# Optimization experiments

Hardware: AMD Instinct MI355X
Metric: run time of the kernel (lower is better)

Reference implementation:

```python
import jax, jax.numpy as jnp
import numpy as np

BSZ, L, P, H = 8, 8192, 128, 128


def setup_inputs() -> dict:
    key = jax.random.key(0)
    ks = jax.random.split(key, 7)
    x = jax.random.normal(ks[0], (BSZ, L, H), jnp.float32)
    A_diag = jax.random.uniform(ks[1], (P,), jnp.float32, 0.0, 2.0)
    G_diag = jax.random.uniform(ks[2], (P,), jnp.float32, 0.0, 1.0)
    dt = jax.random.normal(ks[3], (P,), jnp.float32)
    B = jax.random.uniform(ks[4], (P, H, 2), jnp.float32, -1.0, 1.0) / np.sqrt(H)
    C = jax.random.uniform(ks[5], (H, P, 2), jnp.float32, -1.0, 1.0) / np.sqrt(P)
    D = jax.random.normal(ks[6], (H,), jnp.float32)
    return {"x": x, "A_diag": A_diag, "G_diag": G_diag, "dt": dt, "B": B, "C": C, "D": D}


def _project_G(G, A, dt):
    # clamp G >= 0 and fold A into the valid stability interval [A_low, A_high]
    G = jnp.maximum(G, 0.0)
    dt2 = jnp.maximum(dt ** 2, 1e-06)
    s = jnp.sqrt(1.0 + dt * G)
    A_low = (2.0 + dt * G - 2.0 * s) / dt2
    A_high = (2.0 + dt * G + 2.0 * s) / dt2
    A_proj = A_low + jax.nn.relu(A - A_low) - jax.nn.relu(A - A_high)
    return A_proj, G


def _binop(q_i, q_j):
    # 2x2 block (per diagonal state p) recurrence composition: M_j @ M_i
    A_i, b_i = q_i
    A_j, b_j = q_j
    A_new = jnp.einsum('...ikp,...kjp->...ijp', A_j, A_i)
    b_new = jnp.einsum('...ikp,...kp->...ip', A_j, b_i) + b_j
    return A_new, b_new


def reference(x, A_diag, G_diag, dt, B, C, D):
    # _project_A_dt
    dt_s = jax.nn.sigmoid(dt)                       # (P,)
    A = jnp.maximum(A_diag, 0.0)
    # G_base = projected G given (A, dt)
    _, G_base = _project_G(G_diag, A, dt_s)
    # constant damping: G_seq is G_base broadcast over time, then re-projected per step
    G_seq = jnp.broadcast_to(G_base, (L, P))        # (L,P)
    A_seq, G_seq = _project_G(G_seq, A, dt_s)       # broadcasts over L
    A_fin = jnp.min(A_seq, axis=0)                  # (P,)
    # complex input projection Bu_k = B_complex @ u_k
    Bc = B[..., 0] + 1j * B[..., 1]                 # (P,H)
    Cc = C[..., 0] + 1j * C[..., 1]                 # (H,P)
    Bu = jnp.einsum('blh,ph->blp', x, Bc)           # (BSZ,L,P) complex64
    # IMEX transition coefficients
    S = 1.0 + dt_s * G_seq                          # (L,P)
    M11 = 1.0 / S
    M12 = -(dt_s / S) * A_fin
    M21 = dt_s / S
    M22 = 1.0 - (dt_s ** 2 / S) * A_fin
    M = jnp.stack([jnp.stack([M11, M12], axis=-2),
                   jnp.stack([M21, M22], axis=-2)], axis=-3)   # (L,2,2,P) real
    F = jnp.stack([(dt_s / S) * Bu, (dt_s ** 2 / S) * Bu], axis=-2)  # (BSZ,L,2,P) complex
    M_b = jnp.broadcast_to(M, (BSZ,) + M.shape)     # (BSZ,L,2,2,P)
    _, xs = jax.lax.associative_scan(_binop, (M_b, F), axis=1)
    ys = xs[..., 1, :]                              # (BSZ,L,P) complex: x-component
    out = jnp.einsum('blp,hp->blh', ys, Cc).real + D * x
    return out
```

## Files before the change

### kernel.cpp

```cpp
#include <hip/hip_runtime.h>
#include <math.h>

#define BSZ_ 8
#define LEN_ 8192
#define NC_  256
#define CT_  32

typedef __attribute__((ext_vector_type(8))) short bf16x8;
typedef __attribute__((ext_vector_type(4))) float f32x4;
typedef __attribute__((ext_vector_type(4))) unsigned short u16x4;
typedef __attribute__((ext_vector_type(8))) unsigned short u16x8;

#define OFF_PRM 0
#define OFF_W1T 2048
#define OFF_W2T (OFF_W1T + 16384)
#define OFF_MPW (OFF_W2T + 16384)
#define OFF_SUM (OFF_MPW + 8192)
#define OFF_V2  (OFF_SUM + 1048576)

__device__ __forceinline__ unsigned short f2bf(float f) {
    unsigned u = __builtin_bit_cast(unsigned, f);
    u += 0x7fffu + ((u >> 16) & 1u);
    return (unsigned short)(u >> 16);
}

__device__ __forceinline__ unsigned short f2bf_fast(float f) {
    unsigned u = __builtin_bit_cast(unsigned, f);
    return (unsigned short)((u + 0x8000u) >> 16);
}

__device__ __forceinline__ float bf2f(unsigned short u) {
    return __builtin_bit_cast(float, (unsigned)u << 16);
}

__global__ __launch_bounds__(256) void k_setup(const float* __restrict__ A_diag,
                                               const float* __restrict__ G_diag,
                                               const float* __restrict__ dt,
                                               const float* __restrict__ B,
                                               const float* __restrict__ C,
                                               float* __restrict__ ws)
{
    int i = blockIdx.x * 256 + threadIdx.x;
    {
        int pc = i >> 7, h = i & 127;
        int p = pc >> 1, cc = pc & 1;
        float dts = 1.f / (1.f + expf(-dt[p]));
        float G = fmaxf(G_diag[p], 0.f);
        float c1 = dts / (1.f + dts * G);
        ((unsigned short*)(ws + OFF_W1T))[i] = f2bf(c1 * B[p * 256 + h * 2 + cc]);
    }
    {
        float v = C[i];
        ((unsigned short*)(ws + OFF_W2T))[i] = f2bf((i & 1) ? -v : v);
    }
    if (i < 4096) {
        int k = (i >> 7) + 1;
        int p = i & 127;
        float dtv = dt[p];
        float dts = 1.f / (1.f + expf(-dtv));
        float A   = fmaxf(A_diag[p], 0.f);
        float G   = fmaxf(G_diag[p], 0.f);
        float dt2 = fmaxf(dts * dts, 1e-6f);
        float s   = sqrtf(1.f + dts * G);
        float A_low  = (2.f + dts * G - 2.f * s) / dt2;
        float A_high = (2.f + dts * G + 2.f * s) / dt2;
        float Af = A_low + fmaxf(A - A_low, 0.f) - fmaxf(A - A_high, 0.f);
        float S   = 1.f + dts * G;
        float M11 = 1.f / S;
        float M12 = -(dts / S) * Af;
        float M21 = dts / S;
        float M22 = 1.f - (dts * dts / S) * Af;

        float r11 = 1.f, r12 = 0.f, r21 = 0.f, r22 = 1.f;
        float b11 = M11, b12 = M12, b21 = M21, b22 = M22;
        int kk = k;
#pragma unroll
        for (int it = 0; it < 6; ++it) {
            if (kk & 1) {
                float t11 = b11 * r11 + b12 * r21;
                float t12 = b11 * r12 + b12 * r22;
                float t21 = b21 * r11 + b22 * r21;
                float t22 = b21 * r12 + b22 * r22;
                r11 = t11; r12 = t12; r21 = t21; r22 = t22;
            }
            float s11 = b11 * b11 + b12 * b21;
            float s12 = b11 * b12 + b12 * b22;
            float s21 = b21 * b11 + b22 * b21;
            float s22 = b21 * b12 + b22 * b22;
            b11 = s11; b12 = s12; b21 = s21; b22 = s22;
            kk >>= 1;
        }
        {
            int tq = (k - 1) >> 2, j = (k - 1) & 3;
            ((float2*)(ws + OFF_MPW))[((size_t)tq * 128 + p) * 4 + j] =
                make_float2(r21, r22);
        }

        float* prm = ws + OFF_PRM + p * 16;
        if (k == 1) {
            prm[0] = M11; prm[1] = M12; prm[2] = M21; prm[3] = M22; prm[4] = dts;
        }
        if (k == 32) {
            prm[5] = r11; prm[6] = r12; prm[7] = r21; prm[8] = r22;
            float u11 = r11, u12 = r12, u21 = r21, u22 = r22;
#pragma unroll
            for (int it = 0; it < 4; ++it) {
                float s11 = u11 * u11 + u12 * u21;
                float s12 = u11 * u12 + u12 * u22;
                float s21 = u21 * u11 + u22 * u21;
                float s22 = u21 * u12 + u22 * u22;
                u11 = s11; u12 = s12; u21 = s21; u22 = s22;
            }
            prm[9] = u11; prm[10] = u12; prm[11] = u21; prm[12] = u22;
        }
    }
}

__device__ __forceinline__ void stage_x32(const float* __restrict__ X, size_t row0,
                                          int tid, unsigned short (*xs)[136])
{
    int r = tid >> 4, cl = (tid & 15) * 8;
#pragma unroll
    for (int i = 0; i < 2; ++i) {
        int rr = r + i * 16;
        const float* src = X + (row0 + rr) * 128 + cl;
        float4 v0 = *(const float4*)src;
        float4 v1 = *(const float4*)(src + 4);
        u16x8 pk;
        pk[0] = f2bf_fast(v0.x); pk[1] = f2bf_fast(v0.y);
        pk[2] = f2bf_fast(v0.z); pk[3] = f2bf_fast(v0.w);
        pk[4] = f2bf_fast(v1.x); pk[5] = f2bf_fast(v1.y);
        pk[6] = f2bf_fast(v1.z); pk[7] = f2bf_fast(v1.w);
        *(u16x8*)&xs[rr][cl] = pk;
    }
}

__device__ __forceinline__ void gemm1_acc32(const unsigned short (*xs)[136],
                                            const unsigned short* __restrict__ W1T,
                                            int wv, int lane, f32x4 acc[2][4])
{
    int l15 = lane & 15, quad = lane >> 4;
    int nbase = wv * 64;
#pragma unroll
    for (int kk = 0; kk < 4; ++kk) {
        int k0 = kk * 32 + quad * 8;
        bf16x8 af[2], bg[4];
#pragma unroll
        for (int mi = 0; mi < 2; ++mi) af[mi] = *(const bf16x8*)&xs[mi * 16 + l15][k0];
#pragma unroll
        for (int nj = 0; nj < 4; ++nj)
            bg[nj] = *(const bf16x8*)(W1T + (size_t)(nbase + nj * 16 + l15) * 128 + k0);
#pragma unroll
        for (int mi = 0; mi < 2; ++mi)
#pragma unroll
            for (int nj = 0; nj < 4; ++nj)
                acc[mi][nj] = __builtin_amdgcn_mfma_f32_16x16x32_bf16(af[mi], bg[nj], acc[mi][nj], 0, 0, 0);
    }
}

__global__ __launch_bounds__(256) void k_fuse1(const float* __restrict__ X,
                                               float* __restrict__ ws)
{
    __shared__ __align__(16) char smem[16 * 260 * 4];
    unsigned short (*xs)[136] = (unsigned short (*)[136])smem;
    float (*fl)[260] = (float (*)[260])smem;

    int tid = threadIdx.x;
    int bc = blockIdx.x;
    int b = bc >> 8, c = bc & 255;
    size_t row0 = (size_t)b * LEN_ + (size_t)c * CT_;

    stage_x32(X, row0, tid, xs);
    __syncthreads();

    int wv = tid >> 6, lane = tid & 63;
    int l15 = lane & 15, quad = lane >> 4, nbase = wv * 64;
    f32x4 acc[2][4] = {};
    gemm1_acc32(xs, (const unsigned short*)(ws + OFF_W1T), wv, lane, acc);
    __syncthreads();

    const float* prm = ws + OFF_PRM + (tid >> 1) * 16;
    float M11 = prm[0], M12 = prm[1], dts = prm[4];
    u16x4* V2q = (u16x4*)(ws + OFF_V2) + (size_t)bc * 2048;
    float h1 = 0.f, h2 = 0.f;

#pragma unroll
    for (int half = 0; half < 2; ++half) {
#pragma unroll
        for (int nj = 0; nj < 4; ++nj)
#pragma unroll
            for (int r = 0; r < 4; ++r)
                fl[quad * 4 + r][nbase + nj * 16 + l15] = acc[half][nj][r];
        __syncthreads();
#pragma unroll
        for (int g = 0; g < 4; ++g) {
            u16x4 pk;
#pragma unroll
            for (int i = 0; i < 4; ++i) {
                float u = fl[g * 4 + i][tid];
                float n1 = fmaf(M11, h1, fmaf(M12, h2, u));
                float n2 = fmaf(dts, n1, h2);
                h1 = n1; h2 = n2;
                pk[i] = f2bf_fast(h2);
            }
            V2q[(half * 4 + g) * 256 + tid] = pk;
        }
        __syncthreads();
    }
    *(float2*)(ws + OFF_SUM + ((size_t)bc * 256 + tid) * 2) = make_float2(h1, h2);
}

__global__ __launch_bounds__(256) void k_scan2(float* __restrict__ ws)
{
    __shared__ float2 sums[16][16];
    int blk = blockIdx.x;
    int b = blk >> 4, chb = (blk & 15) * 16;
    int tid = threadIdx.x;
    int chl = tid & 15, seg = tid >> 4;
    int ch = chb + chl;
    const float* prm = ws + OFF_PRM + (ch >> 1) * 16;
    float T11 = prm[5], T12 = prm[6], T21 = prm[7], T22 = prm[8];
    float U11 = prm[9], U12 = prm[10], U21 = prm[11], U22 = prm[12];
    float* base = ws + OFF_SUM + (size_t)b * (NC_ * 512) + ch * 2;

    float l1[16], l2[16];
    float s1 = 0.f, s2 = 0.f;
#pragma unroll
    for (int j = 0; j < 16; ++j) {
        float2 l = *(const float2*)(base + (size_t)(seg * 16 + j) * 512);
        l1[j] = l.x; l2[j] = l.y;
        float n1 = fmaf(T11, s1, fmaf(T12, s2, l.x));
        float n2 = fmaf(T21, s1, fmaf(T22, s2, l.y));
        s1 = n1; s2 = n2;
    }
    sums[chl][seg] = make_float2(s1, s2);
    __syncthreads();

    if (tid < 16) {
        float e1 = 0.f, e2 = 0.f;
#pragma unroll
        for (int k = 0; k < 16; ++k) {
            float2 t = sums[tid][k];
            sums[tid][k] = make_float2(e1, e2);
            float n1 = fmaf(U11, e1, fmaf(U12, e2, t.x));
            float n2 = fmaf(U21, e1, fmaf(U22, e2, t.y));
            e1 = n1; e2 = n2;
        }
    }
    __syncthreads();

    float2 E = sums[chl][seg];
    float e1 = E.x, e2 = E.y;
#pragma unroll
    for (int j = 0; j < 16; ++j) {
        *(float2*)(base + (size_t)(seg * 16 + j) * 512) = make_float2(e1, e2);
        float n1 = fmaf(T11, e1, fmaf(T12, e2, l1[j]));
        float n2 = fmaf(T21, e1, fmaf(T22, e2, l2[j]));
        e1 = n1; e2 = n2;
    }
}

__global__ __launch_bounds__(256) void k_fuse2(const float* __restrict__ X,
                                               const float* __restrict__ Dv,
                                               float* __restrict__ ws,
                                               float* __restrict__ out)
{
    __shared__ __align__(16) unsigned short ysb[32][264];

    int tid = threadIdx.x;
    int bc = blockIdx.x;
    int b = bc >> 8, c = bc & 255;
    size_t row0 = (size_t)b * LEN_ + (size_t)c * CT_;

    {
        int q = tid & 127;
        int tseg = tid >> 7;
        float4 Cp = *(const float4*)(ws + OFF_SUM + ((size_t)bc * 256 + 2 * q) * 2);
        const unsigned short* V2b = (const unsigned short*)(ws + OFF_V2) +
                                    (size_t)bc * 8192;
        const float2* MPW = (const float2*)(ws + OFF_MPW);
#pragma unroll
        for (int g = 0; g < 4; ++g) {
            int tq = tseg * 4 + g;
            u16x8 v = *(const u16x8*)(V2b + (size_t)tq * 1024 + 8 * q);
            const float2* MP = MPW + ((size_t)tq * 128 + q) * 4;
            float4 mA = *(const float4*)MP;
            float4 mB = *(const float4*)(MP + 2);
            int t0 = tq * 4;
            float y0, y1;
            y0 = fmaf(mA.x, Cp.x, fmaf(mA.y, Cp.y, bf2f(v[0])));
            y1 = fmaf(mA.x, Cp.z, fmaf(mA.y, Cp.w, bf2f(v[4])));
            *(ushort2*)&ysb[t0 + 0][2 * q] = make_ushort2(f2bf_fast(y0), f2bf_fast(y1));
            y0 = fmaf(mA.z, Cp.x, fmaf(mA.w, Cp.y, bf2f(v[1])));
            y1 = fmaf(mA.z, Cp.z, fmaf(mA.w, Cp.w, bf2f(v[5])));
            *(ushort2*)&ysb[t0 + 1][2 * q] = make_ushort2(f2bf_fast(y0), f2bf_fast(y1));
            y0 = fmaf(mB.x, Cp.x, fmaf(mB.y, Cp.y, bf2f(v[2])));
            y1 = fmaf(mB.x, Cp.z, fmaf(mB.y, Cp.w, bf2f(v[6])));
            *(ushort2*)&ysb[t0 + 2][2 * q] = make_ushort2(f2bf_fast(y0), f2bf_fast(y1));
            y0 = fmaf(mB.z, Cp.x, fmaf(mB.w, Cp.y, bf2f(v[3])));
            y1 = fmaf(mB.z, Cp.z, fmaf(mB.w, Cp.w, bf2f(v[7])));
            *(ushort2*)&ysb[t0 + 3][2 * q] = make_ushort2(f2bf_fast(y0), f2bf_fast(y1));
        }
    }
    __syncthreads();

    int wv = tid >> 6, lane = tid & 63;
    int l15 = lane & 15, quad = lane >> 4;
    int mrow = (wv & 1) * 16, ncol = (wv >> 1) * 64;
    f32x4 a2[4] = {};
    const unsigned short* W2T = (const unsigned short*)(ws + OFF_W2T);
#pragma unroll
    for (int kk = 0; kk < 8; ++kk) {
        int k0 = kk * 32 + quad * 8;
        bf16x8 af = *(const bf16x8*)&ysb[mrow + l15][k0];
        bf16x8 bg[4];
#pragma unroll
        for (int nj = 0; nj < 4; ++nj)
            bg[nj] = *(const bf16x8*)(W2T + (size_t)(ncol + nj * 16 + l15) * 256 + k0);
#pragma unroll
        for (int nj = 0; nj < 4; ++nj)
            a2[nj] = __builtin_amdgcn_mfma_f32_16x16x32_bf16(af, bg[nj], a2[nj], 0, 0, 0);
    }

#pragma unroll
    for (int nj = 0; nj < 4; ++nj) {
        int col = ncol + nj * 16 + l15;
        float d = Dv[col];
#pragma unroll
        for (int r = 0; r < 4; ++r) {
            size_t gr = row0 + mrow + quad * 4 + r;
            float xv = X[gr * 128 + col];
            out[gr * 128 + col] = fmaf(d, xv, a2[nj][r]);
        }
    }
}

extern "C" void kernel_launch(void* const* d_in, const int* in_sizes, int n_in,
                              void* d_out, int out_size, void* d_ws, size_t ws_size,
                              hipStream_t stream) {
    const float* x      = (const float*)d_in[0];
    const float* A_diag = (const float*)d_in[1];
    const float* G_diag = (const float*)d_in[2];
    const float* dt     = (const float*)d_in[3];
    const float* B      = (const float*)d_in[4];
    const float* C      = (const float*)d_in[5];
    const float* Dv     = (const float*)d_in[6];
    float* out = (float*)d_out;
    float* ws  = (float*)d_ws;

    k_setup<<<128, 256, 0, stream>>>(A_diag, G_diag, dt, B, C, ws);
    k_fuse1<<<BSZ_ * NC_, 256, 0, stream>>>(x, ws);
    k_scan2<<<128, 256, 0, stream>>>(ws);
    k_fuse2<<<BSZ_ * NC_, 256, 0, stream>>>(x, Dv, ws, out);
}
```

Measured before the change: 155.4 us.

## Fuse chunk-scan pipeline into one cooperative kernel with grid syncs

Replaces the three launches (GEMM1 + chunk scan, cross-chunk scan, scan apply + GEMM2) with a single cooperative kernel of 1024 blocks that uses grid.sync between phases. Each block handles 64 rows and keeps the GEMM1 accumulators in registers across the grid barrier, so the intermediate that k_fuse2 reloaded no longer makes a round trip through global memory. This removes launch gaps and intermediate traffic. The cost is two grid-wide barriers, heavier register pressure from holding two accumulator sets under launch_bounds(256,4), and the recurrence being recomputed in phase three. A fallback to the old three-kernel path runs if the cooperative launch fails.

Measured after the change: 433.3 us. 2.79x slower.

```diff
diff --git a/kernel.cpp b/kernel.cpp
--- a/kernel.cpp
+++ b/kernel.cpp
@@ -1,5 +1,8 @@
 #include <hip/hip_runtime.h>
+#include <hip/hip_cooperative_groups.h>
 #include <math.h>
+
+namespace cg = cooperative_groups;
 
 #define BSZ_ 8
 #define LEN_ 8192
@@ -95,7 +98,6 @@
             ((float2*)(ws + OFF_MPW))[((size_t)tq * 128 + p) * 4 + j] =
                 make_float2(r21, r22);
         }
-
         float* prm = ws + OFF_PRM + p * 16;
         if (k == 1) {
             prm[0] = M11; prm[1] = M12; prm[2] = M21; prm[3] = M22; prm[4] = dts;
@@ -158,6 +160,185 @@
     }
 }
 
+__device__ __forceinline__ void gemm2_epi(const unsigned short (*ysb)[264],
+                                          const unsigned short* __restrict__ W2T,
+                                          const float* __restrict__ X,
+                                          const float* __restrict__ Dv,
+                                          float* __restrict__ out,
+                                          size_t rowbase, int wv, int lane)
+{
+    int l15 = lane & 15, quad = lane >> 4;
+    int mrow = (wv & 1) * 16, ncol = (wv >> 1) * 64;
+    f32x4 a2[4] = {};
+#pragma unroll
+    for (int kk = 0; kk < 8; ++kk) {
+        int k0 = kk * 32 + quad * 8;
+        bf16x8 af = *(const bf16x8*)&ysb[mrow + l15][k0];
+        bf16x8 bg[4];
+#pragma unroll
+        for (int nj = 0; nj < 4; ++nj)
+            bg[nj] = *(const bf16x8*)(W2T + (size_t)(ncol + nj * 16 + l15) * 256 + k0);
+#pragma unroll
+        for (int nj = 0; nj < 4; ++nj)
+            a2[nj] = __builtin_amdgcn_mfma_f32_16x16x32_bf16(af, bg[nj], a2[nj], 0, 0, 0);
+    }
+#pragma unroll
+    for (int nj = 0; nj < 4; ++nj) {
+        int col = ncol + nj * 16 + l15;
+        float d = Dv[col];
+#pragma unroll
+        for (int r = 0; r < 4; ++r) {
+            size_t gr = rowbase + mrow + quad * 4 + r;
+            float xv = X[gr * 128 + col];
+            out[gr * 128 + col] = fmaf(d, xv, a2[nj][r]);
+        }
+    }
+}
+
+__global__ __launch_bounds__(256, 4) void k_coop(const float* __restrict__ X,
+                                                 const float* __restrict__ Dv,
+                                                 float* __restrict__ ws,
+                                                 float* __restrict__ out)
+{
+    __shared__ __align__(16) char sm1[17408];
+    __shared__ __align__(16) unsigned short ysb[32][264];
+    __shared__ float2 sums[16][16];
+
+    cg::grid_group grid = cg::this_grid();
+
+    int tid = threadIdx.x;
+    int bid = blockIdx.x;
+    int b = bid >> 7, cb = bid & 127;
+    size_t row0 = (size_t)b * LEN_ + (size_t)cb * 64;
+    int wv = tid >> 6, lane = tid & 63;
+    int l15 = lane & 15, quad = lane >> 4;
+
+    unsigned short (*xs)[136] = (unsigned short (*)[136])sm1;
+    float (*fw)[68] = (float (*)[68])(sm1 + wv * 4352);
+
+    const float* prm = ws + OFF_PRM + (tid >> 1) * 16;
+    float M11 = prm[0], M12 = prm[1], dts = prm[4];
+
+    f32x4 acc0[2][4] = {}, acc1[2][4] = {};
+
+#define SCAN_SUM(ACC, S1, S2)                                              \
+    {                                                                      \
+        float h1 = 0.f, h2 = 0.f;                                          \
+        _Pragma("unroll") for (int half = 0; half < 2; ++half) {           \
+            _Pragma("unroll") for (int nj = 0; nj < 4; ++nj)               \
+                _Pragma("unroll") for (int r = 0; r < 4; ++r)              \
+                    fw[quad * 4 + r][nj * 16 + l15] = ACC[half][nj][r];    \
+            _Pragma("unroll") for (int t = 0; t < 16; ++t) {               \
+                float u = fw[t][lane];                                     \
+                float n1 = fmaf(M11, h1, fmaf(M12, h2, u));                \
+                float n2 = fmaf(dts, n1, h2);                              \
+                h1 = n1; h2 = n2;                                          \
+            }                                                              \
+        }                                                                  \
+        S1 = h1; S2 = h2;                                                  \
+    }
+
+    stage_x32(X, row0, tid, xs);
+    __syncthreads();
+    gemm1_acc32(xs, (const unsigned short*)(ws + OFF_W1T), wv, lane, acc0);
+    __syncthreads();
+    float s01, s02, s11, s12;
+    SCAN_SUM(acc0, s01, s02);
+    __syncthreads();
+    stage_x32(X, row0 + 32, tid, xs);
+    __syncthreads();
+    gemm1_acc32(xs, (const unsigned short*)(ws + OFF_W1T), wv, lane, acc1);
+    __syncthreads();
+    SCAN_SUM(acc1, s11, s12);
+    *(float2*)(ws + OFF_SUM + (((size_t)b * NC_ + 2 * cb) * 256 + tid) * 2) =
+        make_float2(s01, s02);
+    *(float2*)(ws + OFF_SUM + (((size_t)b * NC_ + 2 * cb + 1) * 256 + tid) * 2) =
+        make_float2(s11, s12);
+
+    grid.sync();
+
+    if (bid < 128) {
+        int b2 = bid >> 4, chb = (bid & 15) * 16;
+        int chl = tid & 15, seg = tid >> 4;
+        int ch = chb + chl;
+        const float* pr2 = ws + OFF_PRM + (ch >> 1) * 16;
+        float T11 = pr2[5], T12 = pr2[6], T21 = pr2[7], T22 = pr2[8];
+        float U11 = pr2[9], U12 = pr2[10], U21 = pr2[11], U22 = pr2[12];
+        float* base = ws + OFF_SUM + (size_t)b2 * (NC_ * 512) + ch * 2;
+
+        float s1 = 0.f, s2 = 0.f;
+#pragma unroll
+        for (int j = 0; j < 16; ++j) {
+            float2 l = *(const float2*)(base + (size_t)(seg * 16 + j) * 512);
+            float n1 = fmaf(T11, s1, fmaf(T12, s2, l.x));
+            float n2 = fmaf(T21, s1, fmaf(T22, s2, l.y));
+            s1 = n1; s2 = n2;
+        }
+        sums[chl][seg] = make_float2(s1, s2);
+        __syncthreads();
+        if (tid < 16) {
+            float e1 = 0.f, e2 = 0.f;
+#pragma unroll
+            for (int k = 0; k < 16; ++k) {
+                float2 t = sums[tid][k];
+                sums[tid][k] = make_float2(e1, e2);
+                float n1 = fmaf(U11, e1, fmaf(U12, e2, t.x));
+                float n2 = fmaf(U21, e1, fmaf(U22, e2, t.y));
+                e1 = n1; e2 = n2;
+            }
+        }
+        __syncthreads();
+        float2 E = sums[chl][seg];
+        float e1 = E.x, e2 = E.y;
+#pragma unroll
+        for (int j = 0; j < 16; ++j) {
+            float2 l = *(const float2*)(base + (size_t)(seg * 16 + j) * 512);
+            *(float2*)(base + (size_t)(seg * 16 + j) * 512) = make_float2(e1, e2);
+            float n1 = fmaf(T11, e1, fmaf(T12, e2, l.x));
+            float n2 = fmaf(T21, e1, fmaf(T22, e2, l.y));
+            e1 = n1; e2 = n2;
+        }
+    }
+
+    grid.sync();
+
+    const float2* MPW = (const float2*)(ws + OFF_MPW);
+    int p = tid >> 1;
+    const unsigned short* W2T = (const unsigned short*)(ws + OFF_W2T);
+
+#define PHASE3(ACC, CIDX)                                                  \
+    {                                                                      \
+        float2 Cp = *(const float2*)(ws + OFF_SUM +                        \
+                     (((size_t)b * NC_ + (CIDX)) * 256 + tid) * 2);        \
+        float h1 = 0.f, h2 = 0.f;                                          \
+        _Pragma("unroll") for (int half = 0; half < 2; ++half) {           \
+            _Pragma("unroll") for (int nj = 0; nj < 4; ++nj)               \
+                _Pragma("unroll") for (int r = 0; r < 4; ++r)              \
+                    fw[quad * 4 + r][nj * 16 + l15] = ACC[half][nj][r];    \
+            _Pragma("unroll") for (int t = 0; t < 16; ++t) {               \
+                int tt = half * 16 + t;                                    \
+                float u = fw[t][lane];                                     \
+                float n1 = fmaf(M11, h1, fmaf(M12, h2, u));                \
+                float n2 = fmaf(dts, n1, h2);                              \
+                h1 = n1; h2 = n2;                                          \
+                float2 m = MPW[((size_t)(tt >> 2) * 128 + p) * 4 + (tt & 3)]; \
+                float y = fmaf(m.x, Cp.x, fmaf(m.y, Cp.y, n2));            \
+                ysb[tt][tid] = f2bf_fast(y);                               \
+            }                                                              \
+        }                                                                  \
+    }
+
+    PHASE3(acc0, 2 * cb);
+    __syncthreads();
+    gemm2_epi(ysb, W2T, X, Dv, out, row0, wv, lane);
+    __syncthreads();
+    PHASE3(acc1, 2 * cb + 1);
+    __syncthreads();
+    gemm2_epi(ysb, W2T, X, Dv, out, row0 + 32, wv, lane);
+#undef SCAN_SUM
+#undef PHASE3
+}
+
 __global__ __launch_bounds__(256) void k_fuse1(const float* __restrict__ X,
                                                float* __restrict__ ws)
 {
@@ -235,7 +416,6 @@
     }
     sums[chl][seg] = make_float2(s1, s2);
     __syncthreads();
-
     if (tid < 16) {
         float e1 = 0.f, e2 = 0.f;
 #pragma unroll
@@ -248,7 +428,6 @@
         }
     }
     __syncthreads();
-
     float2 E = sums[chl][seg];
     float e1 = E.x, e2 = E.y;
 #pragma unroll
@@ -305,34 +484,7 @@
     __syncthreads();
 
     int wv = tid >> 6, lane = tid & 63;
-    int l15 = lane & 15, quad = lane >> 4;
-    int mrow = (wv & 1) * 16, ncol = (wv >> 1) * 64;
-    f32x4 a2[4] = {};
-    const unsigned short* W2T = (const unsigned short*)(ws + OFF_W2T);
-#pragma unroll
-    for (int kk = 0; kk < 8; ++kk) {
-        int k0 = kk * 32 + quad * 8;
-        bf16x8 af = *(const bf16x8*)&ysb[mrow + l15][k0];
-        bf16x8 bg[4];
-#pragma unroll
-        for (int nj = 0; nj < 4; ++nj)
-            bg[nj] = *(const bf16x8*)(W2T + (size_t)(ncol + nj * 16 + l15) * 256 + k0);
-#pragma unroll
-        for (int nj = 0; nj < 4; ++nj)
-            a2[nj] = __builtin_amdgcn_mfma_f32_16x16x32_bf16(af, bg[nj], a2[nj], 0, 0, 0);
-    }
-
-#pragma unroll
-    for (int nj = 0; nj < 4; ++nj) {
-        int col = ncol + nj * 16 + l15;
-        float d = Dv[col];
-#pragma unroll
-        for (int r = 0; r < 4; ++r) {
-            size_t gr = row0 + mrow + quad * 4 + r;
-            float xv = X[gr * 128 + col];
-            out[gr * 128 + col] = fmaf(d, xv, a2[nj][r]);
-        }
-    }
+    gemm2_epi(ysb, (const unsigned short*)(ws + OFF_W2T), X, Dv, out, row0, wv, lane);
 }
 
 extern "C" void kernel_launch(void* const* d_in, const int* in_sizes, int n_in,
@@ -349,7 +501,15 @@
     float* ws  = (float*)d_ws;
 
     k_setup<<<128, 256, 0, stream>>>(A_diag, G_diag, dt, B, C, ws);
-    k_fuse1<<<BSZ_ * NC_, 256, 0, stream>>>(x, ws);
-    k_scan2<<<128, 256, 0, stream>>>(ws);
-    k_fuse2<<<BSZ_ * NC_, 256, 0, stream>>>(x, Dv, ws, out);
-}
+
+    const float* Xa = x; const float* Da = Dv; float* wsa = ws; float* outa = out;
+    void* kargs[] = { (void*)&Xa, (void*)&Da, (void*)&wsa, (void*)&outa };
+    hipError_t err = hipLaunchCooperativeKernel((void*)k_coop, dim3(1024), dim3(256),
+                                                kargs, 0, stream);
+    if (err != hipSuccess) {
+        (void)hipGetLastError();
+        k_fuse1<<<BSZ_ * NC_, 256, 0, stream>>>(x, ws);
+        k_scan2<<<128, 256, 0, stream>>>(ws);
+        k_fuse2<<<BSZ_ * NC_, 256, 0, stream>>>(x, Dv, ws, out);
+    }
+}
```
